# Kernel optimization log

Hardware: AMD Instinct MI355X
Metric: run time of the kernel (lower is better)

## Reference

```python
import jax, jax.numpy as jnp
import numpy as np

N_LINKS = 100000
N_EDGES = 1600000
D = 64          # link_state_dim
RU = 256        # readout_units
G = 256         # number of graphs
T = 4           # message passing iterations


def _glorot(key, shape):
    fan_in, fan_out = shape[0], shape[1]
    limit = np.sqrt(6.0 / (fan_in + fan_out)).astype(np.float32)
    return jax.random.uniform(key, shape, jnp.float32, -limit, limit)


def setup_inputs() -> dict:
    key = jax.random.key(0)
    ks = jax.random.split(key, 12)
    states_action = jax.random.normal(ks[0], (N_LINKS, D), jnp.float32)
    states_graph_ids = jnp.sort(jax.random.randint(ks[1], (N_LINKS,), 0, G))
    states_first = jax.random.randint(ks[2], (N_EDGES,), 0, N_LINKS)
    states_second = jax.random.randint(ks[3], (N_EDGES,), 0, N_LINKS)
    # Message: Dense(2D -> D) with selu
    W_msg = _glorot(ks[4], (2 * D, D)); b_msg = jnp.zeros((D,), jnp.float32)
    # GCN: Linear(D -> D) + relu, then unsorted_segment_sum
    W_gcn = _glorot(ks[5], (D, D)); b_gcn = jnp.zeros((D,), jnp.float32)
    # Readout MLP: D -> RU -> RU -> 1
    W_r1 = _glorot(ks[6], (D, RU)); b_r1 = jnp.zeros((RU,), jnp.float32)
    W_r2 = _glorot(ks[7], (RU, RU)); b_r2 = jnp.zeros((RU,), jnp.float32)
    W_r3 = _glorot(ks[8], (RU, 1)); b_r3 = jnp.zeros((1,), jnp.float32)
    return {
        "states_action": states_action,
        "W_msg": W_msg, "b_msg": b_msg,
        "W_gcn": W_gcn, "b_gcn": b_gcn,
        "W_r1": W_r1, "b_r1": b_r1,
        "W_r2": W_r2, "b_r2": b_r2,
        "W_r3": W_r3, "b_r3": b_r3,
        "states_graph_ids": states_graph_ids,
        "states_first": states_first,
        "states_second": states_second,
        "sates_num_edges": N_EDGES,
    }


def reference(states_action, W_msg, b_msg, W_gcn, b_gcn,
              W_r1, b_r1, W_r2, b_r2, W_r3, b_r3,
              states_graph_ids, states_first, states_second, sates_num_edges):
    n_links = states_action.shape[0]
    link_state = states_action
    for _ in range(T):
        main_e = link_state[states_first]      # [E, D]
        neigh_e = link_state[states_second]    # [E, D]
        concat = jnp.concatenate([main_e, neigh_e], axis=1)  # [E, 2D]
        msg = jax.nn.selu(concat @ W_msg + b_msg)            # [E, D]
        h = jax.nn.relu(msg @ W_gcn + b_gcn)                 # [E, D]
        # scatter-add messages back onto links (segment ids = states_second)
        link_state = jax.ops.segment_sum(h, states_second, num_segments=n_links)
        # dropout rate is 0.0 -> identity
    # per-graph readout (graph ids are sorted, fixed G segments)
    graph_emb = jax.ops.segment_sum(link_state, states_graph_ids, num_segments=G)
    r = jax.nn.selu(graph_emb @ W_r1 + b_r1)
    r = jax.nn.selu(r @ W_r2 + b_r2)
    r = r @ W_r3 + b_r3                                      # [G, 1]
    return r
```

## Files before the change

### kernel.cpp

```cpp
#include <hip/hip_runtime.h>
#include <hip/hip_bf16.h>
#include <math.h>

#define D 64
#define RU 256
#define CHUNK 8
#define QSTRIDE 68
#define BIN_SHIFT 7
#define NSB 256

#if __has_builtin(__builtin_amdgcn_exp2f)
#define EXP2F(x) __builtin_amdgcn_exp2f(x)
#else
#define EXP2F(x) exp2f(x)
#endif

typedef short bf16x8 __attribute__((ext_vector_type(8)));
typedef float f32x4 __attribute__((ext_vector_type(4)));

__device__ __forceinline__ float selu_f(float x) {
    return x > 0.0f ? 1.0507009873554805f * x
                    : 1.7580993408473766f * (__expf(x) - 1.0f);
}

__device__ __forceinline__ float selu_x2(float x2) {
    const float p = fmaxf(x2, 0.0f);
    const float n = fminf(x2, 0.0f);
    const float e = EXP2F(n);
    return fmaf(1.7580993408473766f, e, fmaf(0.72829042516f, p, -1.7580993408473766f));
}

__device__ __forceinline__ short f2bf_rtne(float x) {
    union { float f; unsigned u; } v; v.f = x;
    unsigned r = (v.u + 0x7FFFu + ((v.u >> 16) & 1u)) >> 16;
    return (short)r;
}
__device__ __forceinline__ float bf2f(short s) {
    union { float f; unsigned u; } v; v.u = ((unsigned)(unsigned short)s) << 16;
    return v.f;
}
__device__ __forceinline__ unsigned packpair(float a, float b) {
    float2 p; p.x = a; p.y = b;
    __hip_bfloat162 hb = __float22bfloat162_rn(p);
    return *(unsigned*)&hb;
}

__device__ __forceinline__ bf16x8 pack8(const float* v) {
    union { bf16x8 v; unsigned u[4]; } H;
#pragma unroll
    for (int j = 0; j < 4; ++j) H.u[j] = packpair(v[2 * j], v[2 * j + 1]);
    return H.v;
}

#define FIDX(ks, jt, qd, m) ((((((ks) * 4 + (jt)) * 4 + (qd)) * 16) + (m)) * 8)

__global__ __launch_bounds__(256) void wprep_kernel(
    const float* __restrict__ W_msg, const float* __restrict__ W_gcn,
    unsigned short* __restrict__ WAh, unsigned short* __restrict__ WAl,
    unsigned short* __restrict__ WBh, unsigned short* __restrict__ WBl,
    unsigned short* __restrict__ WGh)
{
    const float LOG2E = 1.4426950408889634f;
    const int t = blockIdx.x * 256 + threadIdx.x;
    if (t >= 4096) return;
    const int i  = t & 7;
    const int m  = (t >> 3) & 15;
    const int qd = (t >> 7) & 3;
    const int jt = (t >> 9) & 3;
    const int ks = t >> 11;
    const int kk = ks * 32 + qd * 8 + i;
    const int nn = jt * 16 + m;

    float w = W_msg[kk * 64 + nn] * LOG2E;
    short hi = f2bf_rtne(w);
    WAh[t] = (unsigned short)hi;
    WAl[t] = (unsigned short)f2bf_rtne(w - bf2f(hi));

    w = W_msg[(64 + kk) * 64 + nn] * LOG2E;
    hi = f2bf_rtne(w);
    WBh[t] = (unsigned short)hi;
    WBl[t] = (unsigned short)f2bf_rtne(w - bf2f(hi));

    WGh[t] = (unsigned short)f2bf_rtne(W_gcn[kk * 64 + nn]);
}

__global__ __launch_bounds__(256) void s2bf_kernel(
    const float* __restrict__ in, unsigned short* __restrict__ out, int n4)
{
    for (int i = blockIdx.x * 256 + threadIdx.x; i < n4; i += gridDim.x * 256) {
        const float4 v = ((const float4*)in)[i];
        uint2 o;
        o.x = packpair(v.x, v.y);
        o.y = packpair(v.z, v.w);
        ((uint2*)out)[i] = o;
    }
}


__global__ __launch_bounds__(256) void histA_kernel(
    const int* __restrict__ second, int* __restrict__ ghist,
    int n_edges, int nbins)
{
    __shared__ int lhist[1024];
    for (int i = threadIdx.x; i < nbins; i += 256) lhist[i] = 0;
    __syncthreads();
    const int per = (n_edges + gridDim.x - 1) / gridDim.x;
    const int e0 = blockIdx.x * per;
    const int e1 = min(e0 + per, n_edges);
    for (int e = e0 + threadIdx.x; e < e1; e += 256)
        atomicAdd(&lhist[second[e] >> BIN_SHIFT], 1);
    __syncthreads();
    for (int i = threadIdx.x; i < nbins; i += 256)
        ghist[i * gridDim.x + blockIdx.x] = lhist[i];
}

__global__ __launch_bounds__(64) void sumbins_kernel(
    int* __restrict__ ghist, int* __restrict__ btot, int nbins)
{
    const int b = blockIdx.x, tid = threadIdx.x;
    int d[4], p[4];
#pragma unroll
    for (int k = 0; k < 4; ++k) {
        d[k] = ghist[b * NSB + k * 64 + tid];
        p[k] = d[k];
    }
#pragma unroll
    for (int off = 1; off < 64; off <<= 1) {
#pragma unroll
        for (int k = 0; k < 4; ++k) {
            const int t = __shfl_up(p[k], off, 64);
            if (tid >= off) p[k] += t;
        }
    }
    int base = 0;
#pragma unroll
    for (int k = 0; k < 4; ++k) {
        const int tot = __shfl(p[k], 63, 64);
        ghist[b * NSB + k * 64 + tid] = base + p[k] - d[k];
        base += tot;
    }
    if (tid == 63) btot[b] = base;
}

__global__ __launch_bounds__(1024) void scanS_kernel(int* __restrict__ data, int n)
{
    __shared__ int wsum[16], woff[16];
    const int tid = threadIdx.x, wave = tid >> 6, lane = tid & 63;
    const int x = (tid < n) ? data[tid] : 0;
    int v = x;
#pragma unroll
    for (int off = 1; off < 64; off <<= 1) {
        const int t = __shfl_up(v, off, 64);
        if (lane >= off) v += t;
    }
    if (lane == 63) wsum[wave] = v;
    __syncthreads();
    if (wave == 0) {
        int s = (lane < 16) ? wsum[lane] : 0;
#pragma unroll
        for (int off = 1; off < 16; off <<= 1) {
            const int t = __shfl_up(s, off, 64);
            if (lane >= off) s += t;
        }
        if (lane < 16) woff[lane] = s - wsum[lane];
    }
    __syncthreads();
    if (tid < n) data[tid] = woff[wave] + v - x;
}

__global__ __launch_bounds__(256) void scatterC_kernel(
    const int* __restrict__ first, const int* __restrict__ second,
    const int* __restrict__ ghist, const int* __restrict__ btot,
    unsigned* __restrict__ tmp, int n_edges, int nbins)
{
    __shared__ int lcur[1024];
    for (int i = threadIdx.x; i < nbins; i += 256)
        lcur[i] = ghist[i * NSB + blockIdx.x] + btot[i];
    __syncthreads();
    const int per = (n_edges + gridDim.x - 1) / gridDim.x;
    const int e0 = blockIdx.x * per;
    const int e1 = min(e0 + per, n_edges);
    for (int e = e0 + threadIdx.x; e < e1; e += 256) {
        const int s = second[e];
        const int pos = atomicAdd(&lcur[s >> BIN_SHIFT], 1);
        tmp[pos] = (unsigned)first[e] | ((unsigned)(s & 127) << 20);
    }
}

__global__ __launch_bounds__(256) void binsortD_kernel(
    const unsigned* __restrict__ tmp, const int* __restrict__ btot,
    int* __restrict__ sfirst, int* __restrict__ row_ptr,
    int n_edges, int n_links, int nbins)
{
    __shared__ int ldeg[128];
    __shared__ int lpre[128];
    __shared__ int lcur[128];
    const int b = blockIdx.x;
    const int tid = threadIdx.x;
    const int lbase = b << BIN_SHIFT;
    const int nl = min(128, n_links - lbase);
    const int eb = btot[b];
    const int ee = (b + 1 < nbins) ? btot[b + 1] : n_edges;

    if (tid < 128) ldeg[tid] = 0;
    __syncthreads();
    for (int e = eb + tid; e < ee; e += 256)
        atomicAdd(&ldeg[tmp[e] >> 20], 1);
    __syncthreads();
    if (tid < 64) {
        const int d0 = ldeg[tid], d1 = ldeg[64 + tid];
        int p0 = d0, p1 = d1;
#pragma unroll
        for (int off = 1; off < 64; off <<= 1) {
            const int t0 = __shfl_up(p0, off, 64);
            const int t1 = __shfl_up(p1, off, 64);
            if (tid >= off) { p0 += t0; p1 += t1; }
        }
        const int tot0 = __shfl(p0, 63, 64);
        lpre[tid] = p0 - d0;
        lpre[64 + tid] = tot0 + p1 - d1;
    }
    __syncthreads();
    if (tid < nl) row_ptr[lbase + tid] = eb + lpre[tid];
    if (b == nbins - 1 && tid == 0) row_ptr[n_links] = n_edges;
    if (tid < 128) lcur[tid] = lpre[tid];
    __syncthreads();
    for (int e = eb + tid; e < ee; e += 256) {
        const unsigned v = tmp[e];
        const int pos = eb + atomicAdd(&lcur[v >> 20], 1);
        sfirst[pos] = (int)(v & 0x7FFFFFu);
    }
    if (b == 0)
        for (int i = tid; i < 64; i += 256) sfirst[n_edges + i] = 0;
}

__global__ __launch_bounds__(256) void growfind_kernel(
    const int* __restrict__ gid, int* __restrict__ grow, int n_links, int G)
{
    const int g = blockIdx.x * blockDim.x + threadIdx.x;
    if (g > G) return;
    if (g == G) { grow[G] = n_links; return; }
    int lo = 0, hi = n_links;
    while (lo < hi) {
        const int mid = (lo + hi) >> 1;
        if (gid[mid] < g) lo = mid + 1; else hi = mid;
    }
    grow[g] = lo;
}

__global__ __launch_bounds__(256) void p_mfma_kernel(
    const unsigned short* __restrict__ Sb,
    const unsigned short* __restrict__ WAh, const unsigned short* __restrict__ WAl,
    unsigned short* __restrict__ P, int n_links)
{
    const int tid = threadIdx.x;
    const int wave = tid >> 6;
    const int lane = tid & 63;
    const int m = lane & 15;
    const int qd = lane >> 4;

    bf16x8 Bh[2][4], Bl[2][4];
#pragma unroll
    for (int ks = 0; ks < 2; ++ks)
#pragma unroll
        for (int jt = 0; jt < 4; ++jt) {
            const int off = FIDX(ks, jt, qd, m);
            Bh[ks][jt] = *(const bf16x8*)(WAh + off);
            Bl[ks][jt] = *(const bf16x8*)(WAl + off);
        }
    const bf16x8 z = (bf16x8){0, 0, 0, 0, 0, 0, 0, 0};

    const int ngroups = (n_links + 63) >> 6;
    for (int g = blockIdx.x; g < ngroups; g += gridDim.x) {
        const int base = g * 64 + wave * 16;
        const int l = base + m;
        bf16x8 Ah0 = z, Ah1 = z;
        if (l < n_links) {
            Ah0 = *(const bf16x8*)(Sb + (size_t)l * D + qd * 8);
            Ah1 = *(const bf16x8*)(Sb + (size_t)l * D + 32 + qd * 8);
        }
        f32x4 accP[4];
#pragma unroll
        for (int jt = 0; jt < 4; ++jt) {
            accP[jt] = (f32x4){0.f, 0.f, 0.f, 0.f};
            accP[jt] = __builtin_amdgcn_mfma_f32_16x16x32_bf16(Ah0, Bh[0][jt], accP[jt], 0, 0, 0);
            accP[jt] = __builtin_amdgcn_mfma_f32_16x16x32_bf16(Ah0, Bl[0][jt], accP[jt], 0, 0, 0);
            accP[jt] = __builtin_amdgcn_mfma_f32_16x16x32_bf16(Ah1, Bh[1][jt], accP[jt], 0, 0, 0);
            accP[jt] = __builtin_amdgcn_mfma_f32_16x16x32_bf16(Ah1, Bl[1][jt], accP[jt], 0, 0, 0);
        }
#pragma unroll
        for (int r = 0; r < 4; ++r) {
            const int lr = base + qd * 4 + r;
            if (lr < n_links) {
#pragma unroll
                for (int jt = 0; jt < 4; ++jt)
                    P[(size_t)lr * D + jt * 16 + m] =
                        (unsigned short)f2bf_rtne(accP[jt][r]);
            }
        }
    }
}

__global__ __launch_bounds__(256, 4) void edge_link_kernel(
    unsigned short* __restrict__ Sb, const unsigned short* __restrict__ P,
    const int* __restrict__ sfirst, const int* __restrict__ row_ptr,
    const float* __restrict__ b_msg,
    const unsigned short* __restrict__ WBh, const unsigned short* __restrict__ WBl,
    const unsigned short* __restrict__ WGh,
    const float* __restrict__ b_gcn,
    int n_links)
{
    __shared__ float qt[4][CHUNK * QSTRIDE + 4];
    const int tid = threadIdx.x;
    const int wave = tid >> 6;
    const int lane = tid & 63;
    const int m = lane & 15;
    const int qd = lane >> 4;

    const int l0 = (blockIdx.x * 4 + wave) * CHUNK;
    if (l0 >= n_links) return;
    const int nl = min(CHUNK, n_links - l0);

    const float LOG2E = 1.4426950408889634f;
    float bmsgC[4];
#pragma unroll
    for (int jt = 0; jt < 4; ++jt) bmsgC[jt] = b_msg[jt * 16 + m] * LOG2E;

    {
        const bf16x8 z = (bf16x8){0, 0, 0, 0, 0, 0, 0, 0};
        const int l = l0 + m;
        bf16x8 Ah0 = z, Ah1 = z;
        if ((l < n_links) && (m < CHUNK)) {
            Ah0 = *(const bf16x8*)(Sb + (size_t)l * D + qd * 8);
            Ah1 = *(const bf16x8*)(Sb + (size_t)l * D + 32 + qd * 8);
        }
        f32x4 accQ[4];
#pragma unroll
        for (int jt = 0; jt < 4; ++jt) accQ[jt] = (f32x4){0.f, 0.f, 0.f, 0.f};
#pragma unroll
        for (int ks = 0; ks < 2; ++ks) {
            bf16x8 WbH[4], WbL[4];
#pragma unroll
            for (int jt = 0; jt < 4; ++jt) {
                const int off = FIDX(ks, jt, qd, m);
                WbH[jt] = *(const bf16x8*)(WBh + off);
                WbL[jt] = *(const bf16x8*)(WBl + off);
            }
            const bf16x8 A = ks ? Ah1 : Ah0;
#pragma unroll
            for (int jt = 0; jt < 4; ++jt) {
                accQ[jt] = __builtin_amdgcn_mfma_f32_16x16x32_bf16(A, WbH[jt], accQ[jt], 0, 0, 0);
                accQ[jt] = __builtin_amdgcn_mfma_f32_16x16x32_bf16(A, WbL[jt], accQ[jt], 0, 0, 0);
            }
        }
#pragma unroll
        for (int r = 0; r < 4; ++r) {
            const int row = qd * 4 + r;
            if (row < CHUNK) {
#pragma unroll
                for (int jt = 0; jt < 4; ++jt)
                    qt[wave][row * QSTRIDE + jt * 16 + m] = accQ[jt][r] + bmsgC[jt];
            }
        }
    }

    bf16x8 Gh[2][4];
#pragma unroll
    for (int ks = 0; ks < 2; ++ks)
#pragma unroll
        for (int jt = 0; jt < 4; ++jt)
            Gh[ks][jt] = *(const bf16x8*)(WGh + FIDX(ks, jt, qd, m));

    float bias_gcn[4];
#pragma unroll
    for (int jt = 0; jt < 4; ++jt) bias_gcn[jt] = b_gcn[jt * 16 + m];

    const int rpv = row_ptr[l0 + min(lane, nl)];
#define RP(i) __shfl(rpv, (i), 64)
    const int eb = __builtin_amdgcn_readfirstlane(RP(0));
    const int ee = __builtin_amdgcn_readfirstlane(RP(nl));
    if (eb >= ee) {
        for (int i = 0; i < nl; ++i)
            Sb[(size_t)(l0 + i) * D + lane] = 0;
        return;
    }
    const int ntiles = (ee - eb + 15) >> 4;

    int sv0 = sfirst[eb + m];
    int sv1 = sfirst[eb + 16 + m];
    bf16x8 p00, p01;
    {
        const unsigned short* Pr = P + (size_t)(sv0 & 0xFFFFF) * D;
        p00 = *(const bf16x8*)(Pr + qd * 8);
        p01 = *(const bf16x8*)(Pr + 32 + qd * 8);
    }

    int bcur = 0;
    float rsum[4] = {0.f, 0.f, 0.f, 0.f};
    int eo = eb;

    for (int t = 0; t < ntiles; ++t, eo += 16) {
        const int sv2 = sfirst[eo + 32 + m];
        const unsigned short* Pr1 = P + (size_t)(sv1 & 0xFFFFF) * D;
        const bf16x8 p10 = *(const bf16x8*)(Pr1 + qd * 8);
        const bf16x8 p11 = *(const bf16x8*)(Pr1 + 32 + qd * 8);

        const bool valid = (eo + m < ee);
        const int limv = valid ? ((sv0 >> 20) & 7) : 8;
        const int qoff = (valid ? ((sv0 >> 20) & 7) : 0) * QSTRIDE + qd * 8;

        float qb[16];
        *(float4*)&qb[0]  = *(const float4*)&qt[wave][qoff];
        *(float4*)&qb[4]  = *(const float4*)&qt[wave][qoff + 4];
        *(float4*)&qb[8]  = *(const float4*)&qt[wave][qoff + 32];
        *(float4*)&qb[12] = *(const float4*)&qt[wave][qoff + 36];

        float msgA[8];
#pragma unroll
        for (int i = 0; i < 8; ++i)
            msgA[i] = selu_x2(bf2f(p00[i]) + qb[i]);
        const bf16x8 Ah0 = pack8(msgA);
        float msgB[8];
#pragma unroll
        for (int i = 0; i < 8; ++i)
            msgB[i] = selu_x2(bf2f(p01[i]) + qb[8 + i]);
        const bf16x8 Ah1 = pack8(msgB);

        f32x4 acc[4];
#pragma unroll
        for (int jt = 0; jt < 4; ++jt) {
            const float b = bias_gcn[jt];
            acc[jt] = (f32x4){b, b, b, b};
            acc[jt] = __builtin_amdgcn_mfma_f32_16x16x32_bf16(Ah0, Gh[0][jt], acc[jt], 0, 0, 0);
            acc[jt] = __builtin_amdgcn_mfma_f32_16x16x32_bf16(Ah1, Gh[1][jt], acc[jt], 0, 0, 0);
        }

        const int lr0 = __shfl(limv, qd * 4 + 0, 64);
        const int lr1 = __shfl(limv, qd * 4 + 1, 64);
        const int lr2 = __shfl(limv, qd * 4 + 2, 64);
        const int lr3 = __shfl(limv, qd * 4 + 3, 64);

        while (true) {
            const int b0 = bcur;
#pragma unroll
            for (int jt = 0; jt < 4; ++jt) {
                rsum[jt] += fmaxf((lr0 == b0) ? acc[jt][0] : 0.0f, 0.0f);
                rsum[jt] += fmaxf((lr1 == b0) ? acc[jt][1] : 0.0f, 0.0f);
                rsum[jt] += fmaxf((lr2 == b0) ? acc[jt][2] : 0.0f, 0.0f);
                rsum[jt] += fmaxf((lr3 == b0) ? acc[jt][3] : 0.0f, 0.0f);
            }
            if (bcur < nl && RP(bcur + 1) <= eo + 16) {
#pragma unroll
                for (int jt = 0; jt < 4; ++jt) {
                    rsum[jt] += __shfl_xor(rsum[jt], 16, 64);
                    rsum[jt] += __shfl_xor(rsum[jt], 32, 64);
                }
                const float outv = (qd == 0) ? rsum[0] : (qd == 1) ? rsum[1]
                                 : (qd == 2) ? rsum[2] : rsum[3];
                Sb[(size_t)(l0 + bcur) * D + lane] = (unsigned short)f2bf_rtne(outv);
#pragma unroll
                for (int jt = 0; jt < 4; ++jt) rsum[jt] = 0.0f;
                ++bcur;
                if (bcur >= nl) break;
            } else {
                break;
            }
        }

        sv0 = sv1; sv1 = sv2;
        p00 = p10; p01 = p11;
    }

    while (bcur < nl) {
        Sb[(size_t)(l0 + bcur) * D + lane] = 0;
        ++bcur;
    }
#undef RP
}

__global__ __launch_bounds__(256) void gsum8_kernel(
    const unsigned short* __restrict__ Sb, const int* __restrict__ grow,
    float* __restrict__ gemb)
{
    __shared__ float red[4][64];
    const int g = blockIdx.x >> 3;
    const int slice = blockIdx.x & 7;
    const int slot = threadIdx.x >> 6;
    const int j = threadIdx.x & 63;
    const int ls = grow[g], le = grow[g + 1];
    float acc = 0.0f;
    for (int l = ls + slice * 4 + slot; l < le; l += 32)
        acc += bf2f((short)Sb[(size_t)l * D + j]);
    red[slot][j] = acc;
    __syncthreads();
    if (slot == 0)
        atomicAdd(&gemb[g * D + j], red[0][j] + red[1][j] + red[2][j] + red[3][j]);
}

__global__ __launch_bounds__(256) void mlp_kernel(
    const float* __restrict__ gemb,
    const float* __restrict__ W_r1, const float* __restrict__ b_r1,
    const float* __restrict__ W_r2, const float* __restrict__ b_r2,
    const float* __restrict__ W_r3, const float* __restrict__ b_r3,
    float* __restrict__ out)
{
    __shared__ float gl[64];
    __shared__ float row1[RU];
    __shared__ float row2[RU];
    __shared__ float fin[4];
    const int g = blockIdx.x;
    const int tid = threadIdx.x;
    const int slot = tid >> 6;
    const int lane = tid & 63;

    if (tid < 64) gl[tid] = gemb[g * D + tid];
    __syncthreads();

    float a1 = b_r1[tid];
#pragma unroll 8
    for (int k = 0; k < 64; ++k) a1 += gl[k] * W_r1[k * RU + tid];
    row1[tid] = selu_f(a1);
    __syncthreads();

    float a2 = b_r2[tid];
#pragma unroll 8
    for (int k = 0; k < RU; ++k) a2 += row1[k] * W_r2[k * RU + tid];
    row2[tid] = selu_f(a2);
    __syncthreads();

    float p = row2[tid] * W_r3[tid];
#pragma unroll
    for (int off = 32; off >= 1; off >>= 1)
        p += __shfl_down(p, off, 64);
    if (lane == 0) fin[slot] = p;
    __syncthreads();
    if (tid == 0)
        out[g] = fin[0] + fin[1] + fin[2] + fin[3] + b_r3[0];
}

extern "C" void kernel_launch(void* const* d_in, const int* in_sizes, int n_in,
                              void* d_out, int out_size, void* d_ws, size_t ws_size,
                              hipStream_t stream)
{
    const float* states_action = (const float*)d_in[0];
    const float* W_msg = (const float*)d_in[1];
    const float* b_msg = (const float*)d_in[2];
    const float* W_gcn = (const float*)d_in[3];
    const float* b_gcn = (const float*)d_in[4];
    const float* W_r1 = (const float*)d_in[5];
    const float* b_r1 = (const float*)d_in[6];
    const float* W_r2 = (const float*)d_in[7];
    const float* b_r2 = (const float*)d_in[8];
    const float* W_r3 = (const float*)d_in[9];
    const float* b_r3 = (const float*)d_in[10];
    const int* gid = (const int*)d_in[11];
    const int* first = (const int*)d_in[12];
    const int* second = (const int*)d_in[13];

    const int n_links = in_sizes[0] / D;
    const int n_edges = in_sizes[12];
    const int G = out_size;
    const int nbins = (n_links + 127) >> BIN_SHIFT;

    char* ws2 = (char*)d_ws;
    auto alloc = [&](size_t bytes) {
        char* p = ws2; ws2 += (bytes + 63) & ~(size_t)63; return p;
    };
    unsigned short* Sb = (unsigned short*)alloc((size_t)n_links * D * 2);
    unsigned short* Pb = (unsigned short*)alloc((size_t)n_links * D * 2);
    float* gemb = (float*)alloc((size_t)G * D * sizeof(float));
    int* row_ptr = (int*)alloc((size_t)(n_links + 1) * sizeof(int));
    int* grow = (int*)alloc((size_t)(G + 1) * sizeof(int));
    unsigned* tmp = (unsigned*)alloc((size_t)n_edges * sizeof(unsigned));
    int* sfirst = (int*)alloc((size_t)(n_edges + 64) * sizeof(int));
    unsigned short* WAh = (unsigned short*)alloc(4096 * 2);
    unsigned short* WAl = (unsigned short*)alloc(4096 * 2);
    unsigned short* WBh = (unsigned short*)alloc(4096 * 2);
    unsigned short* WBl = (unsigned short*)alloc(4096 * 2);
    unsigned short* WGh = (unsigned short*)alloc(4096 * 2);
    int* btot = (int*)alloc((size_t)nbins * sizeof(int));
    int* ghist = (int*)sfirst;

    hipMemsetAsync(gemb, 0, (size_t)G * D * sizeof(float), stream);
    s2bf_kernel<<<1024, 256, 0, stream>>>(states_action, Sb, n_links * D / 4);
    wprep_kernel<<<16, 256, 0, stream>>>(W_msg, W_gcn, WAh, WAl, WBh, WBl, WGh);
    histA_kernel<<<NSB, 256, 0, stream>>>(second, ghist, n_edges, nbins);
    sumbins_kernel<<<nbins, 64, 0, stream>>>(ghist, btot, nbins);
    scanS_kernel<<<1, 1024, 0, stream>>>(btot, nbins);
    scatterC_kernel<<<NSB, 256, 0, stream>>>(first, second, ghist, btot, tmp,
                                             n_edges, nbins);
    binsortD_kernel<<<nbins, 256, 0, stream>>>(tmp, btot, sfirst, row_ptr,
                                               n_edges, n_links, nbins);
    growfind_kernel<<<2, 256, 0, stream>>>(gid, grow, n_links, G);

    const int edge_blocks = (n_links + 4 * CHUNK - 1) / (4 * CHUNK);
    for (int t = 0; t < 4; ++t) {
        p_mfma_kernel<<<1024, 256, 0, stream>>>(Sb, WAh, WAl, Pb, n_links);
        edge_link_kernel<<<edge_blocks, 256, 0, stream>>>(Sb, Pb, sfirst, row_ptr,
                                                          b_msg, WBh, WBl, WGh,
                                                          b_gcn, n_links);
    }

    gsum8_kernel<<<G * 8, 256, 0, stream>>>(Sb, grow, gemb);
    mlp_kernel<<<G, 256, 0, stream>>>(gemb, W_r1, b_r1, W_r2, b_r2,
                                      W_r3, b_r3, (float*)d_out);
}
```

Baseline: 477.4 us.

## Fuse next-iteration link projection into edge_link epilogue with double-buffered P

Each wave now stages its freshly reduced link-state rows in LDS. It then runs the hi/lo bf16 MFMA projection for the next iteration's P directly in the edge kernel's epilogue, writing to a second P buffer. After the first iteration this drops three separate p_mfma_kernel launches and their extra pass over the link states. In exchange, the edge kernel gains extra LDS, register pressure and weight loads, which may reduce its occupancy. It also needs extra workspace, with a fallback path when that workspace is not available.

```diff
diff --git a/kernel.cpp b/kernel.cpp
--- a/kernel.cpp
+++ b/kernel.cpp
@@ -6,6 +6,7 @@
 #define RU 256
 #define CHUNK 8
 #define QSTRIDE 68
+#define SSTRIDE 72
 #define BIN_SHIFT 7
 #define NSB 256
 
@@ -308,9 +309,12 @@
     const unsigned short* __restrict__ WBh, const unsigned short* __restrict__ WBl,
     const unsigned short* __restrict__ WGh,
     const float* __restrict__ b_gcn,
+    const unsigned short* __restrict__ WAh, const unsigned short* __restrict__ WAl,
+    unsigned short* __restrict__ Pout, int do_p,
     int n_links)
 {
     __shared__ float qt[4][CHUNK * QSTRIDE + 4];
+    __shared__ unsigned short srow[4][CHUNK * SSTRIDE];
     const int tid = threadIdx.x;
     const int wave = tid >> 6;
     const int lane = tid & 63;
@@ -380,8 +384,10 @@
     const int eb = __builtin_amdgcn_readfirstlane(RP(0));
     const int ee = __builtin_amdgcn_readfirstlane(RP(nl));
     if (eb >= ee) {
-        for (int i = 0; i < nl; ++i)
+        for (int i = 0; i < nl; ++i) {
             Sb[(size_t)(l0 + i) * D + lane] = 0;
+            if (do_p) Pout[(size_t)(l0 + i) * D + lane] = 0;
+        }
         return;
     }
     const int ntiles = (ee - eb + 15) >> 4;
@@ -457,7 +463,9 @@
                 }
                 const float outv = (qd == 0) ? rsum[0] : (qd == 1) ? rsum[1]
                                  : (qd == 2) ? rsum[2] : rsum[3];
-                Sb[(size_t)(l0 + bcur) * D + lane] = (unsigned short)f2bf_rtne(outv);
+                const unsigned short sbv = (unsigned short)f2bf_rtne(outv);
+                Sb[(size_t)(l0 + bcur) * D + lane] = sbv;
+                srow[wave][bcur * SSTRIDE + lane] = sbv;
 #pragma unroll
                 for (int jt = 0; jt < 4; ++jt) rsum[jt] = 0.0f;
                 ++bcur;
@@ -473,7 +481,42 @@
 
     while (bcur < nl) {
         Sb[(size_t)(l0 + bcur) * D + lane] = 0;
+        srow[wave][bcur * SSTRIDE + lane] = 0;
         ++bcur;
+    }
+
+    if (do_p) {
+        const bf16x8 z = (bf16x8){0, 0, 0, 0, 0, 0, 0, 0};
+        bf16x8 Sa0 = z, Sa1 = z;
+        if (m < nl) {
+            Sa0 = *(const bf16x8*)&srow[wave][m * SSTRIDE + qd * 8];
+            Sa1 = *(const bf16x8*)&srow[wave][m * SSTRIDE + 32 + qd * 8];
+        }
+        f32x4 accP[4];
+#pragma unroll
+        for (int jt = 0; jt < 4; ++jt) accP[jt] = (f32x4){0.f, 0.f, 0.f, 0.f};
+#pragma unroll
+        for (int ks = 0; ks < 2; ++ks) {
+            const bf16x8 A = ks ? Sa1 : Sa0;
+#pragma unroll
+            for (int jt = 0; jt < 4; ++jt) {
+                const int off = FIDX(ks, jt, qd, m);
+                const bf16x8 BH = *(const bf16x8*)(WAh + off);
+                const bf16x8 BL = *(const bf16x8*)(WAl + off);
+                accP[jt] = __builtin_amdgcn_mfma_f32_16x16x32_bf16(A, BH, accP[jt], 0, 0, 0);
+                accP[jt] = __builtin_amdgcn_mfma_f32_16x16x32_bf16(A, BL, accP[jt], 0, 0, 0);
+            }
+        }
+#pragma unroll
+        for (int r = 0; r < 4; ++r) {
+            const int lr = qd * 4 + r;
+            if (lr < nl) {
+#pragma unroll
+                for (int jt = 0; jt < 4; ++jt)
+                    Pout[(size_t)(l0 + lr) * D + jt * 16 + m] =
+                        (unsigned short)f2bf_rtne(accP[jt][r]);
+            }
+        }
     }
 #undef RP
 }
@@ -581,6 +624,11 @@
     int* btot = (int*)alloc((size_t)nbins * sizeof(int));
     int* ghist = (int*)sfirst;
 
+    const size_t used = (size_t)(ws2 - (char*)d_ws);
+    const size_t p2bytes = (size_t)n_links * D * 2;
+    const bool pfuse = (used + p2bytes + 64 <= ws_size);
+    unsigned short* Pb2 = pfuse ? (unsigned short*)alloc(p2bytes) : Pb;
+
     hipMemsetAsync(gemb, 0, (size_t)G * D * sizeof(float), stream);
     s2bf_kernel<<<1024, 256, 0, stream>>>(states_action, Sb, n_links * D / 4);
     wprep_kernel<<<16, 256, 0, stream>>>(W_msg, W_gcn, WAh, WAl, WBh, WBl, WGh);
@@ -594,11 +642,23 @@
     growfind_kernel<<<2, 256, 0, stream>>>(gid, grow, n_links, G);
 
     const int edge_blocks = (n_links + 4 * CHUNK - 1) / (4 * CHUNK);
-    for (int t = 0; t < 4; ++t) {
-        p_mfma_kernel<<<1024, 256, 0, stream>>>(Sb, WAh, WAl, Pb, n_links);
-        edge_link_kernel<<<edge_blocks, 256, 0, stream>>>(Sb, Pb, sfirst, row_ptr,
-                                                          b_msg, WBh, WBl, WGh,
-                                                          b_gcn, n_links);
+    p_mfma_kernel<<<1024, 256, 0, stream>>>(Sb, WAh, WAl, Pb, n_links);
+    if (pfuse) {
+        unsigned short* Pc = Pb;
+        unsigned short* Pn = Pb2;
+        for (int t = 0; t < 4; ++t) {
+            edge_link_kernel<<<edge_blocks, 256, 0, stream>>>(
+                Sb, Pc, sfirst, row_ptr, b_msg, WBh, WBl, WGh, b_gcn,
+                WAh, WAl, Pn, (t < 3) ? 1 : 0, n_links);
+            unsigned short* sw = Pc; Pc = Pn; Pn = sw;
+        }
+    } else {
+        for (int t = 0; t < 4; ++t) {
+            if (t) p_mfma_kernel<<<1024, 256, 0, stream>>>(Sb, WAh, WAl, Pb, n_links);
+            edge_link_kernel<<<edge_blocks, 256, 0, stream>>>(
+                Sb, Pb, sfirst, row_ptr, b_msg, WBh, WBl, WGh, b_gcn,
+                WAh, WAl, Pb, 0, n_links);
+        }
     }
 
     gsum8_kernel<<<G * 8, 256, 0, stream>>>(Sb, grow, gemb);
```

Measured after the change: 448.9 us. -6.0%, faster.
